# Kernel tuning notes

Hardware: AMD Instinct MI355X
Metric: run time of the kernel (lower is better)

The kernel has to match this reference:

```python
import jax, jax.numpy as jnp
import numpy as np

B, D, H = 65536, 3, 256  # collocation batch, coord dim, hidden width


def setup_inputs() -> dict:
    key = jax.random.key(0)
    ks = jax.random.split(key, 8)

    def init(k, shape, fan_in):
        return jax.random.normal(k, shape, dtype=jnp.float32) * np.float32(1.0 / np.sqrt(fan_in))

    return {
        "x": jax.random.uniform(ks[0], (B, D), dtype=jnp.float32, minval=0.1, maxval=1.0),
        "W0": init(ks[1], (D, H), D), "b0": jnp.zeros((H,), jnp.float32),
        "W1": init(ks[2], (H, H), H), "b1": jnp.zeros((H,), jnp.float32),
        "W2": init(ks[3], (H, H), H), "b2": jnp.zeros((H,), jnp.float32),
        "W3": init(ks[4], (H, H), H), "b3": jnp.zeros((H,), jnp.float32),
        "Wout": init(ks[5], (H, 1), H), "bout": jnp.zeros((1,), jnp.float32),
    }


def reference(x, W0, b0, W1, b1, W2, b2, W3, b3, Wout, bout):
    # Scalar PINN network u(xi), xi: [D]
    def u_fn(xi):
        h = jnp.tanh(xi @ W0 + b0)
        h = jnp.tanh(h @ W1 + b1)
        h = jnp.tanh(h @ W2 + b2)
        h = jnp.tanh(h @ W3 + b3)
        return (h @ Wout + bout)[0]

    u = jax.vmap(u_fn)(x)                               # [B]
    # batch_gradient: du/dx_i for every coordinate axis (Cartesian: no adjustment)
    grads = jax.vmap(jax.grad(u_fn))(x)                 # [B, D]
    # batch_hessian diagonal: d^2u/dx_i^2 via forward-over-reverse
    hess_fn = jax.jacfwd(jax.grad(u_fn))                # [D, D] per sample
    hess_diag = jax.vmap(lambda xi: jnp.diagonal(hess_fn(xi)))(x)  # [B, D]
    # pack (u, grad, hessian-diagonal) as the PDE-residual ingredients
    return jnp.concatenate([u[:, None], grads, hess_diag], axis=1)  # [B, 1+D+D]
```

## Files before the change

### kernel.cpp

```cpp
#include <hip/hip_runtime.h>
#include <hip/hip_fp16.h>

#define HDIM 256
#define MS 16
#define LDAK 264
#define CSTRIDE (MS * LDAK * 2)

typedef _Float16 half8 __attribute__((ext_vector_type(8)));
typedef _Float16 half4 __attribute__((ext_vector_type(4)));
typedef _Float16 half2v __attribute__((ext_vector_type(2)));
typedef float f32x4 __attribute__((ext_vector_type(4)));

__device__ __forceinline__ float fast_tanh(float x) {
    float e = __expf(2.0f * x);
    return 1.0f - 2.0f * __builtin_amdgcn_rcpf(e + 1.0f);
}

__device__ __forceinline__ half4 cvt4(float a, float b, float c, float d) {
    half2v lo = __builtin_bit_cast(half2v, __builtin_amdgcn_cvt_pkrtz(a, b));
    half2v hi = __builtin_bit_cast(half2v, __builtin_amdgcn_cvt_pkrtz(c, d));
    half4 r; r[0] = lo[0]; r[1] = lo[1]; r[2] = hi[0]; r[3] = hi[1];
    return r;
}

__device__ __forceinline__ void barrier_lds() {
    asm volatile("s_waitcnt lgkmcnt(0)\n\ts_barrier" ::: "memory");
}

__global__ __launch_bounds__(256) void pack_weights(const float* __restrict__ W1,
                                                    const float* __restrict__ W2,
                                                    const float* __restrict__ W3,
                                                    _Float16* __restrict__ out) {
    int tid = blockIdx.x * 256 + threadIdx.x;
    int l = tid >> 13;
    int idx = tid & 8191;
    int kg = idx >> 8;
    int n = idx & 255;
    const float* W = (l == 0) ? W1 : (l == 1) ? W2 : W3;
    half8 v;
    #pragma unroll
    for (int j = 0; j < 8; ++j) v[j] = (_Float16)W[(kg * 8 + j) * 256 + n];
    *(half8*)(out + l * 65536 + kg * 2048 + n * 8) = v;
}

__global__ __launch_bounds__(256, 2)
void pinn_fused(const float* __restrict__ x,
                const float* __restrict__ W0,
                const float* __restrict__ b0,
                const float* __restrict__ b1,
                const float* __restrict__ b2,
                const float* __restrict__ b3,
                const float* __restrict__ Wout,
                const float* __restrict__ bout,
                const _Float16* __restrict__ Wp,
                float* __restrict__ out) {
    __shared__ __align__(16) _Float16 Abuf[7 * MS][LDAK];
    __shared__ float part[4 * 7 * MS];

    const int tid  = threadIdx.x;
    const int lane = tid & 63;
    const int wid  = tid >> 6;
    const int qd   = lane >> 4;
    const int n15  = lane & 15;
    const int base = blockIdx.x * MS;
    const int nw   = wid * 64 + n15;

    const int voff0 = (qd * 256 + nw) * 8;

    half8 wf[3][4];
    #pragma unroll
    for (int t = 0; t < 4; ++t)
        wf[0][t] = *(const half8*)(Wp + 0 * 8192 + voff0 + t * 128);
    #pragma unroll
    for (int t = 0; t < 4; ++t)
        wf[1][t] = *(const half8*)(Wp + 1 * 8192 + voff0 + t * 128);

    {
        const int m  = tid & 15;
        const int nb = (tid >> 4) * 16;
        const float x0 = x[(base + m) * 3 + 0];
        const float x1 = x[(base + m) * 3 + 1];
        const float x2 = x[(base + m) * 3 + 2];
        #pragma unroll
        for (int ch = 0; ch < 2; ++ch) {
            const int n0 = nb + ch * 8;
            f32x4 w0v[2], w1v[2], w2v[2], bv[2];
            w0v[0] = *(const f32x4*)(W0 + n0);            w0v[1] = *(const f32x4*)(W0 + n0 + 4);
            w1v[0] = *(const f32x4*)(W0 + HDIM + n0);     w1v[1] = *(const f32x4*)(W0 + HDIM + n0 + 4);
            w2v[0] = *(const f32x4*)(W0 + 2 * HDIM + n0); w2v[1] = *(const f32x4*)(W0 + 2 * HDIM + n0 + 4);
            bv[0]  = *(const f32x4*)(b0 + n0);            bv[1]  = *(const f32x4*)(b0 + n0 + 4);
            half8 h[7];
            #pragma unroll
            for (int r = 0; r < 8; ++r) {
                const float w0 = w0v[r >> 2][r & 3];
                const float w1 = w1v[r >> 2][r & 3];
                const float w2 = w2v[r >> 2][r & 3];
                float z  = x0 * w0 + x1 * w1 + x2 * w2 + bv[r >> 2][r & 3];
                float tv = fast_tanh(z);
                float dd = 1.f - tv * tv;
                float c2 = -2.f * tv * dd;
                h[0][r] = (_Float16)tv;
                h[1][r] = (_Float16)(dd * w0);
                h[2][r] = (_Float16)(dd * w1);
                h[3][r] = (_Float16)(dd * w2);
                h[4][r] = (_Float16)(c2 * w0 * w0);
                h[5][r] = (_Float16)(c2 * w1 * w1);
                h[6][r] = (_Float16)(c2 * w2 * w2);
            }
            #pragma unroll
            for (int c = 0; c < 7; ++c)
                *(half8*)&Abuf[c * MS + m][n0] = h[c];
        }
    }
    barrier_lds();

    const char* Ab = (const char*)Abuf;
    const int abase = (n15 * LDAK + qd * 8) * 2;
    char* Sb = (char*)Abuf;
    const int sbase = (n15 * LDAK + wid * 64 + qd * 4) * 2;

    #pragma unroll
    for (int l = 0; l < 2; ++l) {
        const float* bb = (l == 0) ? b1 : b2;

        f32x4 acc[7][4];
        #pragma unroll
        for (int c = 0; c < 7; ++c)
            #pragma unroll
            for (int t = 0; t < 4; ++t) acc[c][t] = (f32x4){0.f, 0.f, 0.f, 0.f};

        #pragma unroll
        for (int s = 0; s < 8; ++s) {
            const int g = l * 8 + s;
            {
                #pragma unroll
                for (int t = 0; t < 4; ++t)
                    wf[(g + 2) % 3][t] =
                        *(const half8*)(Wp + (g + 2) * 8192 + voff0 + t * 128);
            }
            half8 af[7];
            #pragma unroll
            for (int c = 0; c < 7; ++c)
                af[c] = *(const half8*)(Ab + abase + c * CSTRIDE + s * 64);
            #pragma unroll
            for (int c = 0; c < 7; ++c)
                #pragma unroll
                for (int t = 0; t < 4; ++t)
                    acc[c][t] = __builtin_amdgcn_mfma_f32_16x16x32_f16(wf[g % 3][t], af[c], acc[c][t], 0, 0, 0);
        }
        barrier_lds();

        #pragma unroll
        for (int t = 0; t < 4; ++t) {
            const int ncol = wid * 64 + t * 16 + qd * 4;
            f32x4 bv = *(const f32x4*)(bb + ncol);
            float tv[4], gj[3][4], sj[3][4];
            #pragma unroll
            for (int r = 0; r < 4; ++r) {
                float zv = acc[0][t][r] + bv[r];
                tv[r] = fast_tanh(zv);
                float dd = 1.f - tv[r] * tv[r];
                float c2 = -2.f * tv[r] * dd;
                #pragma unroll
                for (int i = 0; i < 3; ++i) {
                    float zg = acc[1 + i][t][r];
                    float zs = acc[4 + i][t][r];
                    gj[i][r] = dd * zg;
                    sj[i][r] = dd * zs + c2 * zg * zg;
                }
            }
            *(half4*)(Sb + sbase + 0 * CSTRIDE + t * 32) = cvt4(tv[0], tv[1], tv[2], tv[3]);
            #pragma unroll
            for (int i = 0; i < 3; ++i) {
                *(half4*)(Sb + sbase + (1 + i) * CSTRIDE + t * 32) =
                    cvt4(gj[i][0], gj[i][1], gj[i][2], gj[i][3]);
                *(half4*)(Sb + sbase + (4 + i) * CSTRIDE + t * 32) =
                    cvt4(sj[i][0], sj[i][1], sj[i][2], sj[i][3]);
            }
        }
        barrier_lds();
    }

    {
        f32x4 acc[7][4];
        #pragma unroll
        for (int c = 0; c < 7; ++c)
            #pragma unroll
            for (int t = 0; t < 4; ++t) acc[c][t] = (f32x4){0.f, 0.f, 0.f, 0.f};

        #pragma unroll
        for (int s = 0; s < 8; ++s) {
            const int g = 16 + s;
            if (g + 2 < 24) {
                #pragma unroll
                for (int t = 0; t < 4; ++t)
                    wf[(g + 2) % 3][t] =
                        *(const half8*)(Wp + (g + 2) * 8192 + voff0 + t * 128);
            }
            half8 af[7];
            #pragma unroll
            for (int c = 0; c < 7; ++c)
                af[c] = *(const half8*)(Ab + abase + c * CSTRIDE + s * 64);
            #pragma unroll
            for (int c = 0; c < 7; ++c)
                #pragma unroll
                for (int t = 0; t < 4; ++t)
                    acc[c][t] = __builtin_amdgcn_mfma_f32_16x16x32_f16(wf[g % 3][t], af[c], acc[c][t], 0, 0, 0);
        }

        float p[7] = {0.f, 0.f, 0.f, 0.f, 0.f, 0.f, 0.f};
        #pragma unroll
        for (int t = 0; t < 4; ++t) {
            const int ncol = wid * 64 + t * 16 + qd * 4;
            f32x4 bv = *(const f32x4*)(b3 + ncol);
            f32x4 wv = *(const f32x4*)(Wout + ncol);
            #pragma unroll
            for (int r = 0; r < 4; ++r) {
                float zv = acc[0][t][r] + bv[r];
                float tv = fast_tanh(zv);
                float dd = 1.f - tv * tv;
                float c2 = -2.f * tv * dd;
                p[0] += tv * wv[r];
                #pragma unroll
                for (int i = 0; i < 3; ++i) {
                    float zg = acc[1 + i][t][r];
                    float zs = acc[4 + i][t][r];
                    p[1 + i] += (dd * zg) * wv[r];
                    p[4 + i] += (dd * zs + c2 * zg * zg) * wv[r];
                }
            }
        }
        #pragma unroll
        for (int c = 0; c < 7; ++c) {
            p[c] += __shfl_xor(p[c], 16, 64);
            p[c] += __shfl_xor(p[c], 32, 64);
        }
        if (lane < 16) {
            #pragma unroll
            for (int c = 0; c < 7; ++c)
                part[(wid * 7 + c) * MS + lane] = p[c];
        }
    }
    barrier_lds();

    if (tid < 7 * MS) {
        const int c = tid >> 4;
        const int m = tid & 15;
        float v = part[(0 * 7 + c) * MS + m] + part[(1 * 7 + c) * MS + m] +
                  part[(2 * 7 + c) * MS + m] + part[(3 * 7 + c) * MS + m];
        if (c == 0) v += bout[0];
        out[(base + m) * 7 + c] = v;
    }
}

extern "C" void kernel_launch(void* const* d_in, const int* in_sizes, int n_in,
                              void* d_out, int out_size, void* d_ws, size_t ws_size,
                              hipStream_t stream) {
    const float* xp   = (const float*)d_in[0];
    const float* W0   = (const float*)d_in[1];
    const float* b0   = (const float*)d_in[2];
    const float* W1   = (const float*)d_in[3];
    const float* b1   = (const float*)d_in[4];
    const float* W2   = (const float*)d_in[5];
    const float* b2   = (const float*)d_in[6];
    const float* W3   = (const float*)d_in[7];
    const float* b3   = (const float*)d_in[8];
    const float* Wout = (const float*)d_in[9];
    const float* bout = (const float*)d_in[10];
    _Float16* Wp = (_Float16*)d_ws;

    pack_weights<<<96, 256, 0, stream>>>(W1, W2, W3, Wp);
    pinn_fused<<<65536 / MS, 256, 0, stream>>>(xp, W0, b0, b1, b2, b3, Wout, bout, Wp,
                                               (float*)d_out);
}
```

Before: 247.8 us.

## Overlap layer epilogues and layer-0 compute with next layer's MFMA k-steps

Reorders the k-chunks of each hidden-layer GEMM through a permutation so the chunks written by the first half of the previous epilogue are consumed first. This lets half of each tanh/derivative epilogue, and half of the layer-0 expansion, run interleaved with the next layer's MFMA steps, with extra barriers between the halves. The goal is to hide the elementwise and LDS-write latency behind matrix work. In exchange two accumulator sets are live at once, which raises register pressure and risks spilling or lower occupancy.

New measurement: 251.4 us. Within noise of the previous version (+1.4%).

```diff
diff --git a/kernel.cpp b/kernel.cpp
--- a/kernel.cpp
+++ b/kernel.cpp
@@ -67,147 +67,160 @@
 
     const int voff0 = (qd * 256 + nw) * 8;
 
-    half8 wf[3][4];
-    #pragma unroll
-    for (int t = 0; t < 4; ++t)
-        wf[0][t] = *(const half8*)(Wp + 0 * 8192 + voff0 + t * 128);
-    #pragma unroll
-    for (int t = 0; t < 4; ++t)
-        wf[1][t] = *(const half8*)(Wp + 1 * 8192 + voff0 + t * 128);
-
-    {
-        const int m  = tid & 15;
-        const int nb = (tid >> 4) * 16;
-        const float x0 = x[(base + m) * 3 + 0];
-        const float x1 = x[(base + m) * 3 + 1];
-        const float x2 = x[(base + m) * 3 + 2];
-        #pragma unroll
-        for (int ch = 0; ch < 2; ++ch) {
-            const int n0 = nb + ch * 8;
-            f32x4 w0v[2], w1v[2], w2v[2], bv[2];
-            w0v[0] = *(const f32x4*)(W0 + n0);            w0v[1] = *(const f32x4*)(W0 + n0 + 4);
-            w1v[0] = *(const f32x4*)(W0 + HDIM + n0);     w1v[1] = *(const f32x4*)(W0 + HDIM + n0 + 4);
-            w2v[0] = *(const f32x4*)(W0 + 2 * HDIM + n0); w2v[1] = *(const f32x4*)(W0 + 2 * HDIM + n0 + 4);
-            bv[0]  = *(const f32x4*)(b0 + n0);            bv[1]  = *(const f32x4*)(b0 + n0 + 4);
-            half8 h[7];
-            #pragma unroll
-            for (int r = 0; r < 8; ++r) {
-                const float w0 = w0v[r >> 2][r & 3];
-                const float w1 = w1v[r >> 2][r & 3];
-                const float w2 = w2v[r >> 2][r & 3];
-                float z  = x0 * w0 + x1 * w1 + x2 * w2 + bv[r >> 2][r & 3];
-                float tv = fast_tanh(z);
-                float dd = 1.f - tv * tv;
-                float c2 = -2.f * tv * dd;
-                h[0][r] = (_Float16)tv;
-                h[1][r] = (_Float16)(dd * w0);
-                h[2][r] = (_Float16)(dd * w1);
-                h[3][r] = (_Float16)(dd * w2);
-                h[4][r] = (_Float16)(c2 * w0 * w0);
-                h[5][r] = (_Float16)(c2 * w1 * w1);
-                h[6][r] = (_Float16)(c2 * w2 * w2);
-            }
-            #pragma unroll
-            for (int c = 0; c < 7; ++c)
-                *(half8*)&Abuf[c * MS + m][n0] = h[c];
-        }
-    }
-    barrier_lds();
-
     const char* Ab = (const char*)Abuf;
     const int abase = (n15 * LDAK + qd * 8) * 2;
     char* Sb = (char*)Abuf;
     const int sbase = (n15 * LDAK + wid * 64 + qd * 4) * 2;
 
-    #pragma unroll
-    for (int l = 0; l < 2; ++l) {
-        const float* bb = (l == 0) ? b1 : b2;
-
-        f32x4 acc[7][4];
-        #pragma unroll
-        for (int c = 0; c < 7; ++c)
-            #pragma unroll
-            for (int t = 0; t < 4; ++t) acc[c][t] = (f32x4){0.f, 0.f, 0.f, 0.f};
-
-        #pragma unroll
-        for (int s = 0; s < 8; ++s) {
-            const int g = l * 8 + s;
-            {
-                #pragma unroll
-                for (int t = 0; t < 4; ++t)
-                    wf[(g + 2) % 3][t] =
-                        *(const half8*)(Wp + (g + 2) * 8192 + voff0 + t * 128);
-            }
-            half8 af[7];
-            #pragma unroll
-            for (int c = 0; c < 7; ++c)
-                af[c] = *(const half8*)(Ab + abase + c * CSTRIDE + s * 64);
-            #pragma unroll
-            for (int c = 0; c < 7; ++c)
-                #pragma unroll
-                for (int t = 0; t < 4; ++t)
-                    acc[c][t] = __builtin_amdgcn_mfma_f32_16x16x32_f16(wf[g % 3][t], af[c], acc[c][t], 0, 0, 0);
-        }
-        barrier_lds();
-
-        #pragma unroll
-        for (int t = 0; t < 4; ++t) {
-            const int ncol = wid * 64 + t * 16 + qd * 4;
-            f32x4 bv = *(const f32x4*)(bb + ncol);
-            float tv[4], gj[3][4], sj[3][4];
-            #pragma unroll
-            for (int r = 0; r < 4; ++r) {
-                float zv = acc[0][t][r] + bv[r];
-                tv[r] = fast_tanh(zv);
-                float dd = 1.f - tv[r] * tv[r];
-                float c2 = -2.f * tv[r] * dd;
-                #pragma unroll
-                for (int i = 0; i < 3; ++i) {
-                    float zg = acc[1 + i][t][r];
-                    float zs = acc[4 + i][t][r];
-                    gj[i][r] = dd * zg;
-                    sj[i][r] = dd * zs + c2 * zg * zg;
-                }
-            }
-            *(half4*)(Sb + sbase + 0 * CSTRIDE + t * 32) = cvt4(tv[0], tv[1], tv[2], tv[3]);
-            #pragma unroll
-            for (int i = 0; i < 3; ++i) {
-                *(half4*)(Sb + sbase + (1 + i) * CSTRIDE + t * 32) =
-                    cvt4(gj[i][0], gj[i][1], gj[i][2], gj[i][3]);
-                *(half4*)(Sb + sbase + (4 + i) * CSTRIDE + t * 32) =
-                    cvt4(sj[i][0], sj[i][1], sj[i][2], sj[i][3]);
-            }
-        }
-        barrier_lds();
-    }
+    const int perm[8] = {0, 2, 4, 6, 1, 3, 5, 7};
+
+    half8 wf[3][4];
+
+#define PREF(J) do { \
+    if ((J) < 24) { \
+        const int gp_ = (((J) >> 3) * 8) + perm[(J) & 7]; \
+        _Pragma("unroll") \
+        for (int t_ = 0; t_ < 4; ++t_) \
+            wf[(J) % 3][t_] = *(const half8*)(Wp + gp_ * 8192 + voff0 + t_ * 128); \
+    } \
+} while (0)
+
+#define KSTEP(ACC, J) do { \
+    const int s_ = perm[(J) & 7]; \
+    PREF((J) + 2); \
+    half8 af_[7]; \
+    _Pragma("unroll") \
+    for (int c_ = 0; c_ < 7; ++c_) \
+        af_[c_] = *(const half8*)(Ab + abase + c_ * CSTRIDE + s_ * 64); \
+    _Pragma("unroll") \
+    for (int c_ = 0; c_ < 7; ++c_) \
+        _Pragma("unroll") \
+        for (int t_ = 0; t_ < 4; ++t_) \
+            ACC[c_][t_] = __builtin_amdgcn_mfma_f32_16x16x32_f16(wf[(J) % 3][t_], af_[c_], ACC[c_][t_], 0, 0, 0); \
+} while (0)
+
+#define ELEMW(ACC, BB, T) do { \
+    const int ncol_ = wid * 64 + (T) * 16 + qd * 4; \
+    f32x4 bv_ = *(const f32x4*)((BB) + ncol_); \
+    float tv_[4], gj_[3][4], sj_[3][4]; \
+    _Pragma("unroll") \
+    for (int r_ = 0; r_ < 4; ++r_) { \
+        float zv_ = ACC[0][T][r_] + bv_[r_]; \
+        tv_[r_] = fast_tanh(zv_); \
+        float dd_ = 1.f - tv_[r_] * tv_[r_]; \
+        float c2_ = -2.f * tv_[r_] * dd_; \
+        _Pragma("unroll") \
+        for (int i_ = 0; i_ < 3; ++i_) { \
+            float zg_ = ACC[1 + i_][T][r_]; \
+            float zs_ = ACC[4 + i_][T][r_]; \
+            gj_[i_][r_] = dd_ * zg_; \
+            sj_[i_][r_] = dd_ * zs_ + c2_ * zg_ * zg_; \
+        } \
+    } \
+    *(half4*)(Sb + sbase + 0 * CSTRIDE + (T) * 32) = cvt4(tv_[0], tv_[1], tv_[2], tv_[3]); \
+    _Pragma("unroll") \
+    for (int i_ = 0; i_ < 3; ++i_) { \
+        *(half4*)(Sb + sbase + (1 + i_) * CSTRIDE + (T) * 32) = \
+            cvt4(gj_[i_][0], gj_[i_][1], gj_[i_][2], gj_[i_][3]); \
+        *(half4*)(Sb + sbase + (4 + i_) * CSTRIDE + (T) * 32) = \
+            cvt4(sj_[i_][0], sj_[i_][1], sj_[i_][2], sj_[i_][3]); \
+    } \
+} while (0)
+
+#define L0CHUNK(N0) do { \
+    const int n0_ = (N0); \
+    f32x4 w0v_[2], w1v_[2], w2v_[2], b0v_[2]; \
+    w0v_[0] = *(const f32x4*)(W0 + n0_);            w0v_[1] = *(const f32x4*)(W0 + n0_ + 4); \
+    w1v_[0] = *(const f32x4*)(W0 + HDIM + n0_);     w1v_[1] = *(const f32x4*)(W0 + HDIM + n0_ + 4); \
+    w2v_[0] = *(const f32x4*)(W0 + 2 * HDIM + n0_); w2v_[1] = *(const f32x4*)(W0 + 2 * HDIM + n0_ + 4); \
+    b0v_[0] = *(const f32x4*)(b0 + n0_);            b0v_[1] = *(const f32x4*)(b0 + n0_ + 4); \
+    half8 h_[7]; \
+    _Pragma("unroll") \
+    for (int r_ = 0; r_ < 8; ++r_) { \
+        const float w0_ = w0v_[r_ >> 2][r_ & 3]; \
+        const float w1_ = w1v_[r_ >> 2][r_ & 3]; \
+        const float w2_ = w2v_[r_ >> 2][r_ & 3]; \
+        float z_  = x0 * w0_ + x1 * w1_ + x2 * w2_ + b0v_[r_ >> 2][r_ & 3]; \
+        float tv_ = fast_tanh(z_); \
+        float dd_ = 1.f - tv_ * tv_; \
+        float c2_ = -2.f * tv_ * dd_; \
+        h_[0][r_] = (_Float16)tv_; \
+        h_[1][r_] = (_Float16)(dd_ * w0_); \
+        h_[2][r_] = (_Float16)(dd_ * w1_); \
+        h_[3][r_] = (_Float16)(dd_ * w2_); \
+        h_[4][r_] = (_Float16)(c2_ * w0_ * w0_); \
+        h_[5][r_] = (_Float16)(c2_ * w1_ * w1_); \
+        h_[6][r_] = (_Float16)(c2_ * w2_ * w2_); \
+    } \
+    _Pragma("unroll") \
+    for (int c_ = 0; c_ < 7; ++c_) \
+        *(half8*)&Abuf[c_ * MS + m0][n0_] = h_[c_]; \
+} while (0)
+
+    PREF(0);
+    PREF(1);
+
+    const int m0 = tid & 15;
+    const int cidx = tid >> 4;
+    const int n0A = (cidx >> 2) * 64 + (cidx & 3) * 8;
+    const float x0 = x[(base + m0) * 3 + 0];
+    const float x1 = x[(base + m0) * 3 + 1];
+    const float x2 = x[(base + m0) * 3 + 2];
+
+    L0CHUNK(n0A);
+    barrier_lds();
+
+    f32x4 acc1[7][4];
+    #pragma unroll
+    for (int c = 0; c < 7; ++c)
+        #pragma unroll
+        for (int t = 0; t < 4; ++t) acc1[c][t] = (f32x4){0.f, 0.f, 0.f, 0.f};
+
+    KSTEP(acc1, 0);
+    L0CHUNK(n0A + 32);
+    KSTEP(acc1, 1);
+    KSTEP(acc1, 2);
+    KSTEP(acc1, 3);
+    barrier_lds();
+    KSTEP(acc1, 4); KSTEP(acc1, 5); KSTEP(acc1, 6); KSTEP(acc1, 7);
+    ELEMW(acc1, b1, 0);
+    ELEMW(acc1, b1, 1);
+    barrier_lds();
+
+    f32x4 acc2[7][4];
+    #pragma unroll
+    for (int c = 0; c < 7; ++c)
+        #pragma unroll
+        for (int t = 0; t < 4; ++t) acc2[c][t] = (f32x4){0.f, 0.f, 0.f, 0.f};
+
+    KSTEP(acc2, 8);
+    ELEMW(acc1, b1, 2);
+    KSTEP(acc2, 9);
+    KSTEP(acc2, 10);
+    ELEMW(acc1, b1, 3);
+    KSTEP(acc2, 11);
+    barrier_lds();
+    KSTEP(acc2, 12); KSTEP(acc2, 13); KSTEP(acc2, 14); KSTEP(acc2, 15);
+    ELEMW(acc2, b2, 0);
+    ELEMW(acc2, b2, 1);
+    barrier_lds();
+
+    f32x4 acc3[7][4];
+    #pragma unroll
+    for (int c = 0; c < 7; ++c)
+        #pragma unroll
+        for (int t = 0; t < 4; ++t) acc3[c][t] = (f32x4){0.f, 0.f, 0.f, 0.f};
+
+    KSTEP(acc3, 16);
+    ELEMW(acc2, b2, 2);
+    KSTEP(acc3, 17);
+    KSTEP(acc3, 18);
+    ELEMW(acc2, b2, 3);
+    KSTEP(acc3, 19);
+    barrier_lds();
+    KSTEP(acc3, 20); KSTEP(acc3, 21); KSTEP(acc3, 22); KSTEP(acc3, 23);
 
     {
-        f32x4 acc[7][4];
-        #pragma unroll
-        for (int c = 0; c < 7; ++c)
-            #pragma unroll
-            for (int t = 0; t < 4; ++t) acc[c][t] = (f32x4){0.f, 0.f, 0.f, 0.f};
-
-        #pragma unroll
-        for (int s = 0; s < 8; ++s) {
-            const int g = 16 + s;
-            if (g + 2 < 24) {
-                #pragma unroll
-                for (int t = 0; t < 4; ++t)
-                    wf[(g + 2) % 3][t] =
-                        *(const half8*)(Wp + (g + 2) * 8192 + voff0 + t * 128);
-            }
-            half8 af[7];
-            #pragma unroll
-            for (int c = 0; c < 7; ++c)
-                af[c] = *(const half8*)(Ab + abase + c * CSTRIDE + s * 64);
-            #pragma unroll
-            for (int c = 0; c < 7; ++c)
-                #pragma unroll
-                for (int t = 0; t < 4; ++t)
-                    acc[c][t] = __builtin_amdgcn_mfma_f32_16x16x32_f16(wf[g % 3][t], af[c], acc[c][t], 0, 0, 0);
-        }
-
         float p[7] = {0.f, 0.f, 0.f, 0.f, 0.f, 0.f, 0.f};
         #pragma unroll
         for (int t = 0; t < 4; ++t) {
@@ -216,15 +229,15 @@
             f32x4 wv = *(const f32x4*)(Wout + ncol);
             #pragma unroll
             for (int r = 0; r < 4; ++r) {
-                float zv = acc[0][t][r] + bv[r];
+                float zv = acc3[0][t][r] + bv[r];
                 float tv = fast_tanh(zv);
                 float dd = 1.f - tv * tv;
                 float c2 = -2.f * tv * dd;
                 p[0] += tv * wv[r];
                 #pragma unroll
                 for (int i = 0; i < 3; ++i) {
-                    float zg = acc[1 + i][t][r];
-                    float zs = acc[4 + i][t][r];
+                    float zg = acc3[1 + i][t][r];
+                    float zs = acc3[4 + i][t][r];
                     p[1 + i] += (dd * zg) * wv[r];
                     p[4 + i] += (dd * zs + c2 * zg * zg) * wv[r];
                 }
@@ -251,6 +264,11 @@
         if (c == 0) v += bout[0];
         out[(base + m) * 7 + c] = v;
     }
+
+#undef PREF
+#undef KSTEP
+#undef ELEMW
+#undef L0CHUNK
 }
 
 extern "C" void kernel_launch(void* const* d_in, const int* in_sizes, int n_in,
```
